# Kernel tuning notes

Hardware: AMD Instinct MI355X
Metric: run time of the kernel (lower is better)

Reference implementation:

```python
import jax, jax.numpy as jnp
import numpy as np

N_NODES = 50000
N_EDGES = 400000
N_FEAT = 128
HIDDEN = 128
N_HEADS = 4
HEADC = HIDDEN // N_HEADS  # 32
N_CLASSES = 10
K_HOPS = 3
CST = 1e-5


def setup_inputs() -> dict:
    key = jax.random.key(0)
    ks = jax.random.split(key, 12)
    s = 1.0 / np.sqrt(HIDDEN)
    return {
        "node_feat": jax.random.normal(ks[0], (N_NODES, N_FEAT), jnp.float32),
        "edge_index": jax.random.randint(ks[1], (2, N_EDGES), 0, N_NODES, jnp.int64),
        # Linear weights stored as [in, out] so forward is x @ W + b
        "Wt": jax.random.normal(ks[2], (N_FEAT, HIDDEN), jnp.float32) / np.sqrt(N_FEAT),
        "bt": jax.random.normal(ks[3], (HIDDEN,), jnp.float32) * 0.01,
        "Wq": jax.random.normal(ks[4], (HIDDEN, N_HEADS * HEADC), jnp.float32) * s,
        "bq": jax.random.normal(ks[5], (N_HEADS * HEADC,), jnp.float32) * 0.01,
        "Wk": jax.random.normal(ks[6], (HIDDEN, N_HEADS * HEADC), jnp.float32) * s,
        "bk": jax.random.normal(ks[7], (N_HEADS * HEADC,), jnp.float32) * 0.01,
        "Wv": jax.random.normal(ks[8], (HIDDEN, N_HEADS * N_CLASSES), jnp.float32) * s,
        "bv": jax.random.normal(ks[9], (N_HEADS * N_CLASSES,), jnp.float32) * 0.01,
        "hopwise": jnp.ones((K_HOPS + 1,), jnp.float32),          # Parameter(ones(K+1))
        "headwise": jax.random.normal(ks[10], (N_HEADS, K_HOPS), jnp.float32) * 0.1,  # Parameter, zeros at init; randomized for testing
    }


def reference(node_feat, edge_index, Wt, bt, Wq, bq, Wk, bk, Wv, bv, hopwise, headwise):
    N = node_feat.shape[0]
    row, col = edge_index[0], edge_index[1]

    # eval mode: dropout is identity
    x = jax.nn.relu(node_feat @ Wt + bt)                       # [N, hidden]
    Q = (1.0 + jax.nn.elu(x @ Wq + bq)).reshape(N, N_HEADS, HEADC)
    Kf = (1.0 + jax.nn.elu(x @ Wk + bk)).reshape(N, N_HEADS, HEADC)
    V = (x @ Wv + bv).reshape(N, N_HEADS, N_CLASSES)

    M = jnp.einsum('nhi,nhj->nhij', Kf, V)                     # [N, H, headc, C]
    hidden = V * hopwise[0]                                     # ind_gamma & gamma_softmax branch
    layerwise = jax.nn.softmax(headwise, axis=0)                # softmax over heads (dim=-2)

    for hop in range(K_HOPS):
        # PyG sum aggregation, source_to_target: out[col] += x[row]
        M = jax.ops.segment_sum(M[row], col, num_segments=N)
        Kf = jax.ops.segment_sum(Kf[row], col, num_segments=N)
        H = jnp.einsum('nhi,nhij->nhj', Q, M)                  # [N, H, C]
        C = jnp.einsum('nhi,nhi->nh', Q, Kf)[..., None] + CST  # [N, H, 1]
        H = H / C
        gamma = hopwise[hop + 1] * layerwise[:, hop][:, None]  # [H, 1]
        hidden = hidden + gamma * H

    return hidden.sum(axis=-2)                                  # multi_concat=False: sum over heads -> [N, C]
```

## Files before the change

### kernel.cpp

```cpp
#include <hip/hip_runtime.h>
#include <hip/hip_bf16.h>

#define NN 50000
#define NE 400000
#define NF 128
#define HID 128
#define NH 4
#define HC 32
#define NC 10
#define KHOPS 3
#define NBLK ((NN + 1023) / 1024)

typedef unsigned int uint;
typedef unsigned short ushort;
typedef unsigned char uchar;
typedef __attribute__((ext_vector_type(8))) short bf16x8;
typedef __attribute__((ext_vector_type(4))) float f32x4;
typedef __attribute__((ext_vector_type(2))) float f32x2;

__global__ void detect_kernel(const int* __restrict__ ei, int* __restrict__ flag) {
    int w = ei[2 * threadIdx.x + 1];
    unsigned long long b = __ballot(w != 0);
    if (threadIdx.x == 0) *flag = (b == 0ULL) ? 1 : 0;
}

__device__ __forceinline__ int edge_row(const int* ei, int is64, int e) {
    return is64 ? ei[2 * e] : ei[e];
}
__device__ __forceinline__ int edge_col(const int* ei, int is64, int e) {
    return is64 ? ei[2 * NE + 2 * e] : ei[NE + e];
}

__global__ void zero_kernel(int* __restrict__ p, int n) {
    int i = blockIdx.x * blockDim.x + threadIdx.x;
    if (i < n) p[i] = 0;
}

__global__ void hist_kernel(const int* __restrict__ ei, const int* __restrict__ flag,
                            int* __restrict__ counts) {
    int e = blockIdx.x * blockDim.x + threadIdx.x;
    if (e >= NE) return;
    int c = edge_col(ei, *flag, e);
    atomicAdd(&counts[c], 1);
}

__global__ __launch_bounds__(256) void bsum_kernel(const int* __restrict__ counts,
                                                   int* __restrict__ bsum) {
    int b = blockIdx.x, tid = threadIdx.x;
    int base = b * 1024 + tid * 4;
    int4 v = {0, 0, 0, 0};
    if (base < NN) v = *(const int4*)(counts + base);
    int s = v.x + v.y + v.z + v.w;
#pragma unroll
    for (int off = 32; off >= 1; off >>= 1) s += __shfl_xor(s, off);
    __shared__ int ws[4];
    int lane = tid & 63, w = tid >> 6;
    if (lane == 0) ws[w] = s;
    __syncthreads();
    if (tid == 0) bsum[b] = ws[0] + ws[1] + ws[2] + ws[3];
}

__global__ void bscan_kernel(const int* __restrict__ bsum, int* __restrict__ boff,
                             int* __restrict__ rowptr) {
    int lane = threadIdx.x;
    int v = (lane < NBLK) ? bsum[lane] : 0;
    int t = v;
#pragma unroll
    for (int off = 1; off < 64; off <<= 1) {
        int u = __shfl_up(t, off);
        if (lane >= off) t += u;
    }
    if (lane < NBLK) boff[lane] = t - v;
    if (lane == NBLK - 1) rowptr[NN] = t;
}

__global__ __launch_bounds__(256) void scanb_kernel(const int* __restrict__ counts,
                                                    const int* __restrict__ boff,
                                                    int* __restrict__ rowptr,
                                                    int* __restrict__ cursor) {
    int b = blockIdx.x, tid = threadIdx.x;
    int base = b * 1024 + tid * 4;
    int4 v = {0, 0, 0, 0};
    if (base < NN) v = *(const int4*)(counts + base);
    int s3 = v.x + v.y + v.z + v.w;
    int lane = tid & 63, w = tid >> 6;
    int t = s3;
#pragma unroll
    for (int off = 1; off < 64; off <<= 1) {
        int u = __shfl_up(t, off);
        if (lane >= off) t += u;
    }
    __shared__ int ws[4];
    if (lane == 63) ws[w] = t;
    __syncthreads();
    int wofs = boff[b];
    for (int i = 0; i < 4; i++) wofs += (i < w) ? ws[i] : 0;
    int excl = wofs + t - s3;
    if (base < NN) {
        int4 o;
        o.x = excl;
        o.y = excl + v.x;
        o.z = o.y + v.y;
        o.w = o.z + v.z;
        *(int4*)(rowptr + base) = o;
        *(int4*)(cursor + base) = o;
    }
}

__global__ void scatter_kernel(const int* __restrict__ ei, const int* __restrict__ flag,
                               int* __restrict__ cursor, int* __restrict__ srows) {
    int e = blockIdx.x * blockDim.x + threadIdx.x;
    if (e >= NE) return;
    int is64 = *flag;
    int r = edge_row(ei, is64, e);
    int c = edge_col(ei, is64, e);
    int pos = atomicAdd(&cursor[c], 1);
    srows[pos] = r;
}

__device__ __forceinline__ short bfbits(float f) {
    __hip_bfloat16 h = __float2bfloat16(f);
    return *reinterpret_cast<short*>(&h);
}
__device__ __forceinline__ ushort bfbitsu(float f) {
    __hip_bfloat16 h = __float2bfloat16(f);
    return *reinterpret_cast<ushort*>(&h);
}
__device__ __forceinline__ float bfs(ushort u) { return __uint_as_float(((uint)u) << 16); }
__device__ __forceinline__ f32x2 bf2(uint u) {
    return f32x2{__uint_as_float(u << 16), __uint_as_float(u & 0xFFFF0000u)};
}

template<bool HI>
__device__ __forceinline__ uint pk8(float a, float b, uint old) {
    return __builtin_amdgcn_cvt_pk_fp8_f32(a, b, old, HI);
}
template<bool HI>
__device__ __forceinline__ f32x2 upk8(uint w) {
    return __builtin_amdgcn_cvt_pk_f32_fp8(w, HI);
}

__global__ void wconv_kernel(const float* __restrict__ Wt, const float* __restrict__ Wq,
                             const float* __restrict__ Wk, const float* __restrict__ Wv,
                             ushort* __restrict__ Wtb, ushort* __restrict__ Wqkvb) {
    int idx = blockIdx.x * 256 + threadIdx.x;
    if (idx < 128 * 128) {
        int c = idx >> 7, k = idx & 127;
        Wtb[c * 128 + k] = bfbitsu(Wt[k * 128 + c]);
    }
    if (idx < 304 * 128) {
        int c = idx >> 7, k = idx & 127;
        float w;
        if (c < 128) w = Wq[k * 128 + c];
        else if (c < 256) w = Wk[k * 128 + (c - 128)];
        else { int cv = c - 256; w = (cv < 40) ? Wv[k * 40 + cv] : 0.f; }
        Wqkvb[c * 128 + k] = bfbitsu(w);
    }
}

__global__ __launch_bounds__(256) void xm_kernel(const float* __restrict__ nf,
                                                 const ushort* __restrict__ Wtb,
                                                 const float* __restrict__ bt,
                                                 ushort* __restrict__ xb) {
    int wid = threadIdx.x >> 6, lane = threadIdx.x & 63;
    int row0 = blockIdx.x * 64 + wid * 16;
    int r = lane & 15, kg = lane >> 4;
    int ar = row0 + r;
    if (ar > NN - 1) ar = NN - 1;
    int ctbeg = blockIdx.y * 4;
    f32x4 acc[4];
#pragma unroll
    for (int ct = 0; ct < 4; ct++) acc[ct] = f32x4{0.f, 0.f, 0.f, 0.f};
#pragma unroll
    for (int ks = 0; ks < 4; ks++) {
        int k0 = ks * 32 + kg * 8;
        const float4* ap = (const float4*)(nf + (size_t)ar * 128 + k0);
        float4 a0 = ap[0], a1 = ap[1];
        bf16x8 af;
        af[0] = bfbits(a0.x); af[1] = bfbits(a0.y); af[2] = bfbits(a0.z); af[3] = bfbits(a0.w);
        af[4] = bfbits(a1.x); af[5] = bfbits(a1.y); af[6] = bfbits(a1.z); af[7] = bfbits(a1.w);
#pragma unroll
        for (int ct = 0; ct < 4; ct++) {
            bf16x8 bfr = *(const bf16x8*)(Wtb + (size_t)((ctbeg + ct) * 16 + r) * 128 + k0);
            acc[ct] = __builtin_amdgcn_mfma_f32_16x16x32_bf16(af, bfr, acc[ct], 0, 0, 0);
        }
    }
#pragma unroll
    for (int ct = 0; ct < 4; ct++) {
        int c = (ctbeg + ct) * 16 + r;
        float b = bt[c];
#pragma unroll
        for (int reg = 0; reg < 4; reg++) {
            int n = row0 + kg * 4 + reg;
            if (n < NN) {
                float z = acc[ct][reg] + b;
                xb[(size_t)n * 128 + c] = bfbitsu(fmaxf(z, 0.f));
            }
        }
    }
}

template<int CTBEG, int NCT>
__device__ __forceinline__ void qkv_body(const ushort* __restrict__ xb,
                                         const ushort* __restrict__ Wqkvb,
                                         const float* __restrict__ bq,
                                         const float* __restrict__ bk,
                                         const float* __restrict__ bv,
                                         float* __restrict__ Qp,
                                         uchar* __restrict__ K8,
                                         ushort* __restrict__ Vbf,
                                         int row0, int r, int kg) {
    int ar = row0 + r;
    if (ar > NN - 1) ar = NN - 1;
    f32x4 acc[NCT];
#pragma unroll
    for (int ct = 0; ct < NCT; ct++) acc[ct] = f32x4{0.f, 0.f, 0.f, 0.f};
#pragma unroll
    for (int ks = 0; ks < 4; ks++) {
        int k0 = ks * 32 + kg * 8;
        bf16x8 af = *(const bf16x8*)(xb + (size_t)ar * 128 + k0);
#pragma unroll
        for (int ct = 0; ct < NCT; ct++) {
            bf16x8 bfr = *(const bf16x8*)(Wqkvb + (size_t)((CTBEG + ct) * 16 + r) * 128 + k0);
            acc[ct] = __builtin_amdgcn_mfma_f32_16x16x32_bf16(af, bfr, acc[ct], 0, 0, 0);
        }
    }
#pragma unroll
    for (int ct = 0; ct < NCT; ct++) {
        int c = (CTBEG + ct) * 16 + r;
        float bias;
        if (c < 128) bias = bq[c];
        else if (c < 256) bias = bk[c - 128];
        else { int cv = c - 256; bias = (cv < 40) ? bv[cv] : 0.f; }
#pragma unroll
        for (int reg = 0; reg < 4; reg++) {
            int n = row0 + kg * 4 + reg;
            if (n >= NN) continue;
            float z = acc[ct][reg] + bias;
            if (c < 128) {
                float q = z > 0.f ? 1.f + z : __expf(z);
                Qp[(size_t)n * 128 + c] = q;
            } else if (c < 256) {
                int cc = c - 128;
                float kv = (z > 0.f ? 1.f + z : __expf(z)) * 0.0625f;
                uint w = pk8<false>(kv, 0.f, 0u);
                K8[(size_t)n * 128 + cc] = (uchar)(w & 0xFF);
            } else {
                int cv = c - 256;
                if (cv < 40) {
                    int hh = cv / 10, cc = cv - hh * 10;
                    Vbf[(size_t)n * 64 + hh * 16 + cc] = bfbitsu(z);
                }
            }
        }
    }
}

__global__ __launch_bounds__(256) void qkv_kernel(const ushort* __restrict__ xb,
                                                  const ushort* __restrict__ Wqkvb,
                                                  const float* __restrict__ bq,
                                                  const float* __restrict__ bk,
                                                  const float* __restrict__ bv,
                                                  float* __restrict__ Qp,
                                                  uchar* __restrict__ K8,
                                                  ushort* __restrict__ Vbf) {
    int wid = threadIdx.x >> 6, lane = threadIdx.x & 63;
    int row0 = blockIdx.x * 64 + wid * 16;
    int r = lane & 15, kg = lane >> 4;
    if (blockIdx.y == 0)
        qkv_body<0, 8>(xb, Wqkvb, bq, bk, bv, Qp, K8, Vbf, row0, r, kg);
    else if (blockIdx.y == 1)
        qkv_body<8, 8>(xb, Wqkvb, bq, bk, bv, Qp, K8, Vbf, row0, r, kg);
    else
        qkv_body<16, 3>(xb, Wqkvb, bq, bk, bv, Qp, K8, Vbf, row0, r, kg);
}

__global__ __launch_bounds__(256) void aggf0_kernel(const ushort* __restrict__ K8c,
                                                    const ushort* __restrict__ Vbf,
                                                    const float* __restrict__ Qp,
                                                    float* __restrict__ out,
                                                    uint2* __restrict__ Mq2n, ushort* __restrict__ Mr2n,
                                                    uchar* __restrict__ K82n,
                                                    const int* __restrict__ rowptr,
                                                    const int* __restrict__ srows,
                                                    const float* __restrict__ hopwise,
                                                    const float* __restrict__ headwise) {
    int gw = (blockIdx.x * 256 + threadIdx.x) >> 6;
    int lane = threadIdx.x & 63;
    int h = lane >> 4;
    int beg = rowptr[gw], end = rowptr[gw + 1];
    f32x2 A0[5], A1[5], kA = f32x2{0.f, 0.f};
#pragma unroll
    for (int j = 0; j < 5; j++) { A0[j] = f32x2{0.f, 0.f}; A1[j] = f32x2{0.f, 0.f}; }
    int e = beg;
    for (; e + 1 < end; e += 2) {
        int s0 = srows[e], s1 = srows[e + 1];
        uint k0w = K8c[(size_t)s0 * 64 + lane];
        uint k1w = K8c[(size_t)s1 * 64 + lane];
        const ushort* vb0 = Vbf + (size_t)s0 * 64 + h * 16;
        const ushort* vb1 = Vbf + (size_t)s1 * 64 + h * 16;
        uint4 v40 = *(const uint4*)vb0; uint v10 = *(const uint*)(vb0 + 8);
        uint4 v41 = *(const uint4*)vb1; uint v11 = *(const uint*)(vb1 + 8);
        f32x2 kk0 = upk8<false>(k0w);
        f32x2 kk1 = upk8<false>(k1w);
        kA += kk0 + kk1;
        f32x2 V0[5] = {bf2(v40.x), bf2(v40.y), bf2(v40.z), bf2(v40.w), bf2(v10)};
        f32x2 V1[5] = {bf2(v41.x), bf2(v41.y), bf2(v41.z), bf2(v41.w), bf2(v11)};
        f32x2 k00 = f32x2{kk0.x, kk0.x}, k01 = f32x2{kk0.y, kk0.y};
        f32x2 k10 = f32x2{kk1.x, kk1.x}, k11 = f32x2{kk1.y, kk1.y};
#pragma unroll
        for (int j = 0; j < 5; j++) {
            A0[j] += k00 * V0[j] + k10 * V1[j];
            A1[j] += k01 * V0[j] + k11 * V1[j];
        }
    }
    for (; e < end; ++e) {
        int s0 = srows[e];
        uint k0w = K8c[(size_t)s0 * 64 + lane];
        const ushort* vb0 = Vbf + (size_t)s0 * 64 + h * 16;
        uint4 v40 = *(const uint4*)vb0; uint v10 = *(const uint*)(vb0 + 8);
        f32x2 kk0 = upk8<false>(k0w);
        kA += kk0;
        f32x2 V0[5] = {bf2(v40.x), bf2(v40.y), bf2(v40.z), bf2(v40.w), bf2(v10)};
        f32x2 k00 = f32x2{kk0.x, kk0.x}, k01 = f32x2{kk0.y, kk0.y};
#pragma unroll
        for (int j = 0; j < 5; j++) {
            A0[j] += k00 * V0[j];
            A1[j] += k01 * V0[j];
        }
    }
    int p0 = lane * 2;
    float2 q = *(const float2*)(Qp + (size_t)gw * 128 + p0);
    float num[10];
#pragma unroll
    for (int j = 0; j < 5; j++) {
        num[2 * j] = q.x * A0[j].x + q.y * A1[j].x;
        num[2 * j + 1] = q.x * A0[j].y + q.y * A1[j].y;
    }
    float den = q.x * kA.x + q.y * kA.y;
#pragma unroll
    for (int off = 8; off >= 1; off >>= 1) {
#pragma unroll
        for (int c = 0; c < 10; c++) num[c] += __shfl_xor(num[c], off);
        den += __shfl_xor(den, off);
    }
    float e0 = __expf(headwise[0 * KHOPS + 0]);
    float e1 = __expf(headwise[1 * KHOPS + 0]);
    float e2 = __expf(headwise[2 * KHOPS + 0]);
    float e3 = __expf(headwise[3 * KHOPS + 0]);
    float eh = (h == 0) ? e0 : (h == 1) ? e1 : (h == 2) ? e2 : e3;
    float gamma = hopwise[1] * eh / (e0 + e1 + e2 + e3);
    float s = gamma / (den + 6.25e-7f);
    float tot[10];
#pragma unroll
    for (int c = 0; c < 10; c++) {
        tot[c] = s * num[c];
        tot[c] += __shfl_xor(tot[c], 16);
        tot[c] += __shfl_xor(tot[c], 32);
    }
    if (lane < 10) {
        float v = lane == 0 ? tot[0] : lane == 1 ? tot[1] : lane == 2 ? tot[2] :
                  lane == 3 ? tot[3] : lane == 4 ? tot[4] : lane == 5 ? tot[5] :
                  lane == 6 ? tot[6] : lane == 7 ? tot[7] : lane == 8 ? tot[8] : tot[9];
        const ushort* vb = Vbf + (size_t)gw * 64 + lane;
        float vsum = bfs(vb[0]) + bfs(vb[16]) + bfs(vb[32]) + bfs(vb[48]);
        out[(size_t)gw * 10 + lane] = hopwise[0] * vsum + v;
    }
    {
        int R = 2 * gw + (lane >> 5);
        int lp = ((lane >> 4) & 1) * 32 + 2 * (lane & 15);
        uint4 o;
        o.x = pk8<true>(A0[1].x, A0[1].y, pk8<false>(A0[0].x, A0[0].y, 0u));
        o.y = pk8<true>(A0[3].x, A0[3].y, pk8<false>(A0[2].x, A0[2].y, 0u));
        o.z = pk8<true>(A1[1].x, A1[1].y, pk8<false>(A1[0].x, A1[0].y, 0u));
        o.w = pk8<true>(A1[3].x, A1[3].y, pk8<false>(A1[2].x, A1[2].y, 0u));
        *(uint4*)(Mq2n + (size_t)R * 64 + lp) = o;
        uint rw = pk8<true>(A1[4].x, A1[4].y, pk8<false>(A0[4].x, A0[4].y, 0u));
        *(uint*)(Mr2n + (size_t)R * 64 + lp) = rw;
        uint kw = pk8<false>(kA.x, kA.y, 0u);
        *(ushort*)(K82n + (size_t)R * 64 + lp) = (ushort)(kw & 0xFFFF);
    }
}

__device__ __forceinline__ void edge_acc2(f32x2 A[5], float& kA, uint2 m, ushort r, uchar k) {
    A[0] += upk8<false>(m.x);
    A[1] += upk8<true>(m.x);
    A[2] += upk8<false>(m.y);
    A[3] += upk8<true>(m.y);
    A[4] += upk8<false>((uint)r);
    kA += upk8<false>((uint)k).x;
}

__global__ __launch_bounds__(256) void aggf_kernel(const uint2* __restrict__ Mq2,
                                                   const ushort* __restrict__ Mr2,
                                                   const uchar* __restrict__ K82,
                                                   const float* __restrict__ Qp,
                                                   float* __restrict__ out,
                                                   uint2* __restrict__ Mq2n, ushort* __restrict__ Mr2n,
                                                   uchar* __restrict__ K82n,
                                                   const int* __restrict__ rowptr,
                                                   const int* __restrict__ srows,
                                                   const float* __restrict__ hopwise,
                                                   const float* __restrict__ headwise,
                                                   int hop, int write_next) {
    int gwv = (blockIdx.x * 256 + threadIdx.x) >> 6;
    int gw = gwv >> 1;
    int hp = gwv & 1;
    int lane = threadIdx.x & 63;
    int beg = rowptr[gw], end = rowptr[gw + 1];
    f32x2 A[5];
    float kA = 0.f;
#pragma unroll
    for (int j = 0; j < 5; j++) A[j] = f32x2{0.f, 0.f};
    int e = beg;
    for (; e + 3 < end; e += 4) {
        int s0 = srows[e], s1 = srows[e + 1], s2 = srows[e + 2], s3 = srows[e + 3];
        size_t b0 = (size_t)(2 * s0 + hp) * 64 + lane;
        size_t b1 = (size_t)(2 * s1 + hp) * 64 + lane;
        size_t b2 = (size_t)(2 * s2 + hp) * 64 + lane;
        size_t b3 = (size_t)(2 * s3 + hp) * 64 + lane;
        uint2 m0 = Mq2[b0], m1 = Mq2[b1], m2 = Mq2[b2], m3 = Mq2[b3];
        ushort r0 = Mr2[b0], r1 = Mr2[b1], r2 = Mr2[b2], r3 = Mr2[b3];
        uchar k0 = K82[b0], k1 = K82[b1], k2 = K82[b2], k3 = K82[b3];
        edge_acc2(A, kA, m0, r0, k0);
        edge_acc2(A, kA, m1, r1, k1);
        edge_acc2(A, kA, m2, r2, k2);
        edge_acc2(A, kA, m3, r3, k3);
    }
    for (; e < end; ++e) {
        int s0 = srows[e];
        size_t b0 = (size_t)(2 * s0 + hp) * 64 + lane;
        edge_acc2(A, kA, Mq2[b0], Mr2[b0], K82[b0]);
    }
    float q = Qp[(size_t)gw * 128 + hp * 64 + lane];
    float num[10];
#pragma unroll
    for (int j = 0; j < 5; j++) {
        num[2 * j] = q * A[j].x;
        num[2 * j + 1] = q * A[j].y;
    }
    float den = q * kA;
#pragma unroll
    for (int off = 16; off >= 1; off >>= 1) {
#pragma unroll
        for (int c = 0; c < 10; c++) num[c] += __shfl_xor(num[c], off);
        den += __shfl_xor(den, off);
    }
    float e0 = __expf(headwise[0 * KHOPS + hop]);
    float e1 = __expf(headwise[1 * KHOPS + hop]);
    float e2 = __expf(headwise[2 * KHOPS + hop]);
    float e3 = __expf(headwise[3 * KHOPS + hop]);
    int h = hp * 2 + (lane >> 5);
    float eh = (h == 0) ? e0 : (h == 1) ? e1 : (h == 2) ? e2 : e3;
    float gamma = hopwise[hop + 1] * eh / (e0 + e1 + e2 + e3);
    float s = gamma / (den + 6.25e-7f);
    float tot[10];
#pragma unroll
    for (int c = 0; c < 10; c++) {
        tot[c] = s * num[c];
        tot[c] += __shfl_xor(tot[c], 32);
    }
    if (lane < 10) {
        float v = lane == 0 ? tot[0] : lane == 1 ? tot[1] : lane == 2 ? tot[2] :
                  lane == 3 ? tot[3] : lane == 4 ? tot[4] : lane == 5 ? tot[5] :
                  lane == 6 ? tot[6] : lane == 7 ? tot[7] : lane == 8 ? tot[8] : tot[9];
        atomicAdd(&out[(size_t)gw * 10 + lane], v);
    }
    if (write_next) {
        size_t b = (size_t)(2 * gw + hp) * 64 + lane;
        uint2 o;
        o.x = pk8<true>(A[1].x, A[1].y, pk8<false>(A[0].x, A[0].y, 0u));
        o.y = pk8<true>(A[3].x, A[3].y, pk8<false>(A[2].x, A[2].y, 0u));
        Mq2n[b] = o;
        uint rw = pk8<false>(A[4].x, A[4].y, 0u);
        Mr2n[b] = (ushort)(rw & 0xFFFF);
        uint kw = pk8<false>(kA, 0.f, 0u);
        K82n[b] = (uchar)(kw & 0xFF);
    }
}

extern "C" void kernel_launch(void* const* d_in, const int* in_sizes, int n_in,
                              void* d_out, int out_size, void* d_ws, size_t ws_size,
                              hipStream_t stream) {
    const float* nf = (const float*)d_in[0];
    const int* ei = (const int*)d_in[1];
    const float* Wt = (const float*)d_in[2];
    const float* bt = (const float*)d_in[3];
    const float* Wq = (const float*)d_in[4];
    const float* bq = (const float*)d_in[5];
    const float* Wk = (const float*)d_in[6];
    const float* bk = (const float*)d_in[7];
    const float* Wv = (const float*)d_in[8];
    const float* bv = (const float*)d_in[9];
    const float* hopwise = (const float*)d_in[10];
    const float* headwise = (const float*)d_in[11];
    float* out = (float*)d_out;

    char* p = (char*)d_ws;
    auto alloc = [&](size_t bytes) {
        char* r = p;
        p += (bytes + 255) & ~(size_t)255;
        return r;
    };
    int* rowptr = (int*)alloc((NN + 4) * sizeof(int));
    int* cursor = (int*)alloc((NN + 4) * sizeof(int));
    int* bsum = (int*)alloc(NBLK * sizeof(int));
    int* boff = (int*)alloc(NBLK * sizeof(int));
    int* srows = (int*)alloc((size_t)NE * sizeof(int));
    int* flag = (int*)alloc(sizeof(int));
    ushort* Wtb = (ushort*)alloc(128 * 128 * sizeof(ushort));
    ushort* Wqkvb = (ushort*)alloc(304 * 128 * sizeof(ushort));
    float* Qp = (float*)alloc((size_t)NN * 128 * sizeof(float));
    uchar* K8pp = (uchar*)alloc((size_t)NN * 128);
    ushort* Vbf = (ushort*)alloc((size_t)NN * 64 * sizeof(ushort));
    uchar* K82a = (uchar*)alloc((size_t)NN * 128);
    uint2* Mq2a = (uint2*)alloc((size_t)NN * 128 * sizeof(uint2));
    uint2* Mq2b = (uint2*)alloc((size_t)NN * 128 * sizeof(uint2));
    ushort* Mr2a = (ushort*)alloc((size_t)NN * 128 * sizeof(ushort));
    ushort* Mr2b = (ushort*)alloc((size_t)NN * 128 * sizeof(ushort));
    ushort* xb = (ushort*)Mq2a;
    uchar* K82b = K8pp;

    detect_kernel<<<1, 64, 0, stream>>>(ei, flag);
    zero_kernel<<<(NN + 255) / 256, 256, 0, stream>>>(cursor, NN);
    hist_kernel<<<(NE + 255) / 256, 256, 0, stream>>>(ei, flag, cursor);
    bsum_kernel<<<NBLK, 256, 0, stream>>>(cursor, bsum);
    bscan_kernel<<<1, 64, 0, stream>>>(bsum, boff, rowptr);
    scanb_kernel<<<NBLK, 256, 0, stream>>>(cursor, boff, rowptr, cursor);
    scatter_kernel<<<(NE + 255) / 256, 256, 0, stream>>>(ei, flag, cursor, srows);

    wconv_kernel<<<(304 * 128 + 255) / 256, 256, 0, stream>>>(Wt, Wq, Wk, Wv, Wtb, Wqkvb);
    int nrb = (NN + 63) / 64;
    xm_kernel<<<dim3(nrb, 2), 256, 0, stream>>>(nf, Wtb, bt, xb);
    qkv_kernel<<<dim3(nrb, 3), 256, 0, stream>>>(xb, Wqkvb, bq, bk, bv, Qp, K8pp, Vbf);

    aggf0_kernel<<<NN / 4, 256, 0, stream>>>((const ushort*)K8pp, Vbf, Qp, out,
                                             Mq2a, Mr2a, K82a,
                                             rowptr, srows, hopwise, headwise);
    aggf_kernel<<<NN / 2, 256, 0, stream>>>(Mq2a, Mr2a, K82a, Qp, out,
                                            Mq2b, Mr2b, K82b,
                                            rowptr, srows, hopwise, headwise, 1, 1);
    aggf_kernel<<<NN / 2, 256, 0, stream>>>(Mq2b, Mr2b, K82b, Qp, out,
                                            Mq2a, Mr2a, K82a,
                                            rowptr, srows, hopwise, headwise, 2, 0);
}
```

Before: 369.8 us.

## Fuse input MLP and QKV projection into one kernel via shared memory

Merges the x = relu(nf@Wt+bt) kernel with the QKV projection kernel so the hidden activations stay in LDS rather than being written to and re-read from global memory. Each block now computes all 8 hidden column tiles and all 19 QKV tiles itself, instead of splitting them across grid y. It also merges the zero and detect kernels into one launch. The trade-off is fewer blocks with more serial MFMA work and higher register pressure per block, which may reduce occupancy.

Measured after the change: 371.1 us, median of 2. Within noise of the previous version (+0.4%).

```diff
diff --git a/kernel.cpp b/kernel.cpp
--- a/kernel.cpp
+++ b/kernel.cpp
@@ -18,10 +18,15 @@
 typedef __attribute__((ext_vector_type(4))) float f32x4;
 typedef __attribute__((ext_vector_type(2))) float f32x2;
 
-__global__ void detect_kernel(const int* __restrict__ ei, int* __restrict__ flag) {
-    int w = ei[2 * threadIdx.x + 1];
-    unsigned long long b = __ballot(w != 0);
-    if (threadIdx.x == 0) *flag = (b == 0ULL) ? 1 : 0;
+__global__ void zero_detect_kernel(int* __restrict__ p, int n,
+                                   const int* __restrict__ ei, int* __restrict__ flag) {
+    int i = blockIdx.x * blockDim.x + threadIdx.x;
+    if (i < n) p[i] = 0;
+    if (blockIdx.x == 0 && threadIdx.x < 64) {
+        int w = ei[2 * threadIdx.x + 1];
+        unsigned long long b = __ballot(w != 0);
+        if (threadIdx.x == 0) *flag = (b == 0ULL) ? 1 : 0;
+    }
 }
 
 __device__ __forceinline__ int edge_row(const int* ei, int is64, int e) {
@@ -29,11 +34,6 @@
 }
 __device__ __forceinline__ int edge_col(const int* ei, int is64, int e) {
     return is64 ? ei[2 * NE + 2 * e] : ei[NE + e];
-}
-
-__global__ void zero_kernel(int* __restrict__ p, int n) {
-    int i = blockIdx.x * blockDim.x + threadIdx.x;
-    if (i < n) p[i] = 0;
 }
 
 __global__ void hist_kernel(const int* __restrict__ ei, const int* __restrict__ flag,
@@ -158,71 +158,26 @@
     }
 }
 
-__global__ __launch_bounds__(256) void xm_kernel(const float* __restrict__ nf,
-                                                 const ushort* __restrict__ Wtb,
-                                                 const float* __restrict__ bt,
-                                                 ushort* __restrict__ xb) {
-    int wid = threadIdx.x >> 6, lane = threadIdx.x & 63;
-    int row0 = blockIdx.x * 64 + wid * 16;
-    int r = lane & 15, kg = lane >> 4;
-    int ar = row0 + r;
-    if (ar > NN - 1) ar = NN - 1;
-    int ctbeg = blockIdx.y * 4;
-    f32x4 acc[4];
-#pragma unroll
-    for (int ct = 0; ct < 4; ct++) acc[ct] = f32x4{0.f, 0.f, 0.f, 0.f};
+template<int CTBEG, int NCT>
+__device__ __forceinline__ void qkv_stage2(const bf16x8 af2[4],
+                                           const ushort* __restrict__ Wqkvb,
+                                           const float* __restrict__ bq,
+                                           const float* __restrict__ bk,
+                                           const float* __restrict__ bv,
+                                           float* __restrict__ Qp,
+                                           uchar* __restrict__ K8,
+                                           ushort* __restrict__ Vbf,
+                                           int row0, int r, int kg) {
+    f32x4 acc[NCT];
+#pragma unroll
+    for (int ct = 0; ct < NCT; ct++) acc[ct] = f32x4{0.f, 0.f, 0.f, 0.f};
 #pragma unroll
     for (int ks = 0; ks < 4; ks++) {
         int k0 = ks * 32 + kg * 8;
-        const float4* ap = (const float4*)(nf + (size_t)ar * 128 + k0);
-        float4 a0 = ap[0], a1 = ap[1];
-        bf16x8 af;
-        af[0] = bfbits(a0.x); af[1] = bfbits(a0.y); af[2] = bfbits(a0.z); af[3] = bfbits(a0.w);
-        af[4] = bfbits(a1.x); af[5] = bfbits(a1.y); af[6] = bfbits(a1.z); af[7] = bfbits(a1.w);
-#pragma unroll
-        for (int ct = 0; ct < 4; ct++) {
-            bf16x8 bfr = *(const bf16x8*)(Wtb + (size_t)((ctbeg + ct) * 16 + r) * 128 + k0);
-            acc[ct] = __builtin_amdgcn_mfma_f32_16x16x32_bf16(af, bfr, acc[ct], 0, 0, 0);
-        }
-    }
-#pragma unroll
-    for (int ct = 0; ct < 4; ct++) {
-        int c = (ctbeg + ct) * 16 + r;
-        float b = bt[c];
-#pragma unroll
-        for (int reg = 0; reg < 4; reg++) {
-            int n = row0 + kg * 4 + reg;
-            if (n < NN) {
-                float z = acc[ct][reg] + b;
-                xb[(size_t)n * 128 + c] = bfbitsu(fmaxf(z, 0.f));
-            }
-        }
-    }
-}
-
-template<int CTBEG, int NCT>
-__device__ __forceinline__ void qkv_body(const ushort* __restrict__ xb,
-                                         const ushort* __restrict__ Wqkvb,
-                                         const float* __restrict__ bq,
-                                         const float* __restrict__ bk,
-                                         const float* __restrict__ bv,
-                                         float* __restrict__ Qp,
-                                         uchar* __restrict__ K8,
-                                         ushort* __restrict__ Vbf,
-                                         int row0, int r, int kg) {
-    int ar = row0 + r;
-    if (ar > NN - 1) ar = NN - 1;
-    f32x4 acc[NCT];
-#pragma unroll
-    for (int ct = 0; ct < NCT; ct++) acc[ct] = f32x4{0.f, 0.f, 0.f, 0.f};
-#pragma unroll
-    for (int ks = 0; ks < 4; ks++) {
-        int k0 = ks * 32 + kg * 8;
-        bf16x8 af = *(const bf16x8*)(xb + (size_t)ar * 128 + k0);
 #pragma unroll
         for (int ct = 0; ct < NCT; ct++) {
             bf16x8 bfr = *(const bf16x8*)(Wqkvb + (size_t)((CTBEG + ct) * 16 + r) * 128 + k0);
-            acc[ct] = __builtin_amdgcn_mfma_f32_16x16x32_bf16(af, bfr, acc[ct], 0, 0, 0);
+            acc[ct] = __builtin_amdgcn_mfma_f32_16x16x32_bf16(af2[ks], bfr, acc[ct], 0, 0, 0);
         }
     }
 #pragma unroll
@@ -256,7 +211,9 @@
     }
 }
 
-__global__ __launch_bounds__(256) void qkv_kernel(const ushort* __restrict__ xb,
+__global__ __launch_bounds__(256) void mlp_kernel(const float* __restrict__ nf,
+                                                  const ushort* __restrict__ Wtb,
+                                                  const float* __restrict__ bt,
                                                   const ushort* __restrict__ Wqkvb,
                                                   const float* __restrict__ bq,
                                                   const float* __restrict__ bk,
@@ -264,15 +221,48 @@
                                                   float* __restrict__ Qp,
                                                   uchar* __restrict__ K8,
                                                   ushort* __restrict__ Vbf) {
+    __shared__ ushort xs[4][16][136];
     int wid = threadIdx.x >> 6, lane = threadIdx.x & 63;
     int row0 = blockIdx.x * 64 + wid * 16;
     int r = lane & 15, kg = lane >> 4;
-    if (blockIdx.y == 0)
-        qkv_body<0, 8>(xb, Wqkvb, bq, bk, bv, Qp, K8, Vbf, row0, r, kg);
-    else if (blockIdx.y == 1)
-        qkv_body<8, 8>(xb, Wqkvb, bq, bk, bv, Qp, K8, Vbf, row0, r, kg);
-    else
-        qkv_body<16, 3>(xb, Wqkvb, bq, bk, bv, Qp, K8, Vbf, row0, r, kg);
+    int ar = row0 + r;
+    if (ar > NN - 1) ar = NN - 1;
+
+    f32x4 acc[8];
+#pragma unroll
+    for (int ct = 0; ct < 8; ct++) acc[ct] = f32x4{0.f, 0.f, 0.f, 0.f};
+#pragma unroll
+    for (int ks = 0; ks < 4; ks++) {
+        int k0 = ks * 32 + kg * 8;
+        const float4* ap = (const float4*)(nf + (size_t)ar * 128 + k0);
+        float4 a0 = ap[0], a1 = ap[1];
+        bf16x8 af;
+        af[0] = bfbits(a0.x); af[1] = bfbits(a0.y); af[2] = bfbits(a0.z); af[3] = bfbits(a0.w);
+        af[4] = bfbits(a1.x); af[5] = bfbits(a1.y); af[6] = bfbits(a1.z); af[7] = bfbits(a1.w);
+#pragma unroll
+        for (int ct = 0; ct < 8; ct++) {
+            bf16x8 bfr = *(const bf16x8*)(Wtb + (size_t)(ct * 16 + r) * 128 + k0);
+            acc[ct] = __builtin_amdgcn_mfma_f32_16x16x32_bf16(af, bfr, acc[ct], 0, 0, 0);
+        }
+    }
+#pragma unroll
+    for (int ct = 0; ct < 8; ct++) {
+        int c = ct * 16 + r;
+        float b = bt[c];
+#pragma unroll
+        for (int reg = 0; reg < 4; reg++) {
+            float z = acc[ct][reg] + b;
+            xs[wid][kg * 4 + reg][c] = bfbitsu(fmaxf(z, 0.f));
+        }
+    }
+    bf16x8 af2[4];
+#pragma unroll
+    for (int ks = 0; ks < 4; ks++)
+        af2[ks] = *(const bf16x8*)&xs[wid][r][ks * 32 + kg * 8];
+
+    qkv_stage2<0, 8>(af2, Wqkvb, bq, bk, bv, Qp, K8, Vbf, row0, r, kg);
+    qkv_stage2<8, 8>(af2, Wqkvb, bq, bk, bv, Qp, K8, Vbf, row0, r, kg);
+    qkv_stage2<16, 3>(af2, Wqkvb, bq, bk, bv, Qp, K8, Vbf, row0, r, kg);
 }
 
 __global__ __launch_bounds__(256) void aggf0_kernel(const ushort* __restrict__ K8c,
@@ -518,11 +508,9 @@
     uint2* Mq2b = (uint2*)alloc((size_t)NN * 128 * sizeof(uint2));
     ushort* Mr2a = (ushort*)alloc((size_t)NN * 128 * sizeof(ushort));
     ushort* Mr2b = (ushort*)alloc((size_t)NN * 128 * sizeof(ushort));
-    ushort* xb = (ushort*)Mq2a;
     uchar* K82b = K8pp;
 
-    detect_kernel<<<1, 64, 0, stream>>>(ei, flag);
-    zero_kernel<<<(NN + 255) / 256, 256, 0, stream>>>(cursor, NN);
+    zero_detect_kernel<<<(NN + 255) / 256, 256, 0, stream>>>(cursor, NN, ei, flag);
     hist_kernel<<<(NE + 255) / 256, 256, 0, stream>>>(ei, flag, cursor);
     bsum_kernel<<<NBLK, 256, 0, stream>>>(cursor, bsum);
     bscan_kernel<<<1, 64, 0, stream>>>(bsum, boff, rowptr);
@@ -531,8 +519,7 @@
 
     wconv_kernel<<<(304 * 128 + 255) / 256, 256, 0, stream>>>(Wt, Wq, Wk, Wv, Wtb, Wqkvb);
     int nrb = (NN + 63) / 64;
-    xm_kernel<<<dim3(nrb, 2), 256, 0, stream>>>(nf, Wtb, bt, xb);
-    qkv_kernel<<<dim3(nrb, 3), 256, 0, stream>>>(xb, Wqkvb, bq, bk, bv, Qp, K8pp, Vbf);
+    mlp_kernel<<<nrb, 256, 0, stream>>>(nf, Wtb, bt, Wqkvb, bq, bk, bv, Qp, K8pp, Vbf);
 
     aggf0_kernel<<<NN / 4, 256, 0, stream>>>((const ushort*)K8pp, Vbf, Qp, out,
                                              Mq2a, Mr2a, K82a,
```
